# Optimization experiments

Measured on AMD Instinct MI355X. Metric: run time of the kernel, lower is better.

## Reference

```python
import jax, jax.numpy as jnp
import numpy as np

B, S, H = 4, 1024, 1024
NH, HD = 16, 64  # num heads, head dim


def setup_inputs() -> dict:
    key = jax.random.key(0)
    ks = jax.random.split(key, 7)
    scale = 1.0 / np.sqrt(H)
    return {
        "hidden_states": jax.random.normal(ks[0], (B, S, H), jnp.float32),
        "attention_mask": jnp.zeros((B, 1, 1, S), jnp.float32),
        "Wq": jax.random.normal(ks[1], (H, H), jnp.float32) * scale,
        "bq": jnp.zeros((H,), jnp.float32),
        "Wk": jax.random.normal(ks[2], (H, H), jnp.float32) * scale,
        "bk": jnp.zeros((H,), jnp.float32),
        "Wv": jax.random.normal(ks[3], (H, H), jnp.float32) * scale,
        "bv": jnp.zeros((H,), jnp.float32),
    }


def _heads(x):
    # [B,S,H] -> [B,NH,S,HD]
    return x.reshape(x.shape[0], x.shape[1], NH, HD).transpose(0, 2, 1, 3)


def reference(hidden_states, attention_mask, Wq, bq, Wk, bk, Wv, bv):
    q = _heads(hidden_states @ Wq + bq)  # [B,NH,S,HD]
    k = _heads(hidden_states @ Wk + bk)
    v = _heads(hidden_states @ Wv + bv)
    scores = jnp.einsum("bhqd,bhkd->bhqk", q, k) / np.sqrt(HD)
    scores = scores + attention_mask  # broadcast additive mask
    probs = jax.nn.softmax(scores, axis=-1)  # dropout p=0 (eval)
    ctx = jnp.einsum("bhqk,bhkd->bhqd", probs, v)
    # [B,NH,S,HD] -> [B,S,H]
    return ctx.transpose(0, 2, 1, 3).reshape(hidden_states.shape[0], hidden_states.shape[1], NH * HD)
```

## Files before the change

### kernel.cpp

```cpp
#include <hip/hip_runtime.h>
#include <hip/hip_bf16.h>

typedef __bf16 bf16_t;
typedef __bf16 bf16x8 __attribute__((ext_vector_type(8)));
typedef float f32x4 __attribute__((ext_vector_type(4)));
typedef float f32x8 __attribute__((ext_vector_type(8)));
typedef float f32x16 __attribute__((ext_vector_type(16)));
typedef unsigned uint2v __attribute__((ext_vector_type(2)));

#define MFMA16(a, b, c) __builtin_amdgcn_mfma_f32_16x16x32_bf16((a), (b), (c), 0, 0, 0)
#define MFMA32(a, b, c) __builtin_amdgcn_mfma_f32_32x32x16_bf16((a), (b), (c), 0, 0, 0)

static constexpr int BB = 4, SS = 1024, HH = 1024, NHEAD = 16, HDIM = 64;
static constexpr int MM = BB * SS;

__device__ __forceinline__ void gload_lds16(const void* g, void* l) {
  __builtin_amdgcn_global_load_lds((const __attribute__((address_space(1))) void*)g,
                                   (__attribute__((address_space(3))) void*)l, 16, 0, 0);
}

#if __has_builtin(__builtin_amdgcn_permlane32_swap)
#define PSWAP(a, b)                                                    \
  {                                                                    \
    uint2v _r = __builtin_amdgcn_permlane32_swap((a), (b), false, false); \
    (a) = _r.x;                                                        \
    (b) = _r.y;                                                        \
  }
#else
#define PSWAP(a, b) asm("v_permlane32_swap_b32 %0, %1" : "+v"(a), "+v"(b))
#endif

__device__ __forceinline__ float EXP2(float x) {
  float r;
  asm("v_exp_f32 %0, %1" : "=v"(r) : "v"(x));
  return r;
}

__global__ __launch_bounds__(256) void prep_kernel(const float* __restrict__ hs,
                                                   const float* __restrict__ Wq,
                                                   const float* __restrict__ Wk,
                                                   const float* __restrict__ Wv,
                                                   bf16_t* __restrict__ hiddenB,
                                                   bf16_t* __restrict__ WT) {
  const int t = threadIdx.x;
  if (blockIdx.x < 2048) {
    int i = (blockIdx.x * 256 + t) * 8;
    float4 a = *(const float4*)(hs + i);
    float4 b = *(const float4*)(hs + i + 4);
    union { int4 i4; bf16_t h[8]; } u;
    u.h[0] = (bf16_t)a.x; u.h[1] = (bf16_t)a.y; u.h[2] = (bf16_t)a.z; u.h[3] = (bf16_t)a.w;
    u.h[4] = (bf16_t)b.x; u.h[5] = (bf16_t)b.y; u.h[6] = (bf16_t)b.z; u.h[7] = (bf16_t)b.w;
    *(int4*)(hiddenB + i) = u.i4;
  } else {
    __shared__ float tile[32][33];
    int id = blockIdx.x - 2048;
    int z = id >> 10;
    int rem = id & 1023;
    int bx = rem & 31, by = rem >> 5;
    const float* W = (z == 0) ? Wq : (z == 1) ? Wk : Wv;
    bf16_t* Out = WT + (size_t)z * HH * HH;
    int tx = t & 31, ty = t >> 5;
    int x0 = bx * 32;
    int y0 = by * 32;
    for (int j = ty; j < 32; j += 8)
      tile[j][tx] = W[(size_t)(y0 + j) * HH + x0 + tx];
    __syncthreads();
    for (int j = ty; j < 32; j += 8)
      Out[(size_t)(x0 + j) * HH + y0 + tx] = (bf16_t)tile[tx][j];
  }
}

#define BMT 128
#define BNT 384
#define BKT 64
#define NTL 16
#define BUFBYTES 65536

__global__ __launch_bounds__(512, 2) void qkv_gemm3(const bf16_t* __restrict__ hiddenB,
                                                    const bf16_t* __restrict__ WT,
                                                    const float* __restrict__ bq,
                                                    const float* __restrict__ bk,
                                                    const float* __restrict__ bv,
                                                    bf16_t* __restrict__ Qo,
                                                    bf16_t* __restrict__ Ko,
                                                    bf16_t* __restrict__ Vt) {
  __shared__ bf16_t smem[2 * BUFBYTES / 2];

  const int wg = blockIdx.x;
  const int id = (wg & 7) * 32 + (wg >> 3);
  const int nb = id & 7;
  const int mb = id >> 3;

  const int t = threadIdx.x;
  const int lane = t & 63;
  const int w = t >> 6;
  const int wr = w >> 2;
  const int wc = w & 3;
  const int lr = lane & 15;
  const int g4 = lane >> 4;

  const unsigned schunk = (((unsigned)(t & 7)) ^ ((unsigned)((t >> 3) & 7))) << 4;
  const char* Ag = (const char*)hiddenB + (size_t)(mb * BMT) * 2048;
  const char* Bg = (const char*)WT + (size_t)(nb * BNT) * 2048;

  auto stage = [&](const char* gb, int growbase, int kbyte, char* ldsdest) {
    gload_lds16(gb + (size_t)(growbase + (t >> 3)) * 2048 + kbyte + schunk,
                ldsdest + w * 1024);
  };
  auto stage_tile = [&](int kt, char* Sb) {
    const int kb = kt * 128;
    stage(Ag, 0, kb, Sb);
    stage(Ag, 64, kb, Sb + 8192);
#pragma unroll
    for (int i = 0; i < 6; ++i) stage(Bg, i * 64, kb, Sb + 16384 + i * 8192);
  };
  const unsigned axor = ((unsigned)(lr & 7)) << 4;

  f32x4 acc[4][6] = {};

  stage_tile(0, (char*)smem);
  stage_tile(1, (char*)smem + BUFBYTES);
  asm volatile("s_waitcnt vmcnt(8)" ::: "memory");
  __builtin_amdgcn_s_barrier();

  for (int j = 0; j < NTL; ++j) {
    const char* Ab = (const char*)smem + (j & 1) * BUFBYTES;
    const char* Bb = Ab + 16384;

    bf16x8 af[4][2], bfr[6][2];
#pragma unroll
    for (int mi = 0; mi < 4; ++mi)
#pragma unroll
      for (int ks = 0; ks < 2; ++ks)
        af[mi][ks] = *(const bf16x8*)(Ab + (size_t)(wr * 64 + mi * 16 + lr) * 128 +
                                      (((unsigned)(ks * 64 + g4 * 16)) ^ axor));
#pragma unroll
    for (int ni = 0; ni < 6; ++ni)
#pragma unroll
      for (int ks = 0; ks < 2; ++ks)
        bfr[ni][ks] = *(const bf16x8*)(Bb + (size_t)(wc * 96 + ni * 16 + lr) * 128 +
                                       (((unsigned)(ks * 64 + g4 * 16)) ^ axor));

    asm volatile("s_waitcnt lgkmcnt(0)" ::: "memory");
    __builtin_amdgcn_sched_barrier(0);
    __builtin_amdgcn_s_barrier();

    if (j + 2 < NTL) stage_tile(j + 2, (char*)smem + (j & 1) * BUFBYTES);

    __builtin_amdgcn_s_setprio(1);
#pragma unroll
    for (int mi = 0; mi < 4; ++mi)
#pragma unroll
      for (int ni = 0; ni < 6; ++ni)
#pragma unroll
        for (int ks = 0; ks < 2; ++ks)
          acc[mi][ni] = MFMA16(af[mi][ks], bfr[ni][ks], acc[mi][ni]);
    __builtin_amdgcn_s_setprio(0);

    if (j + 1 < NTL) {
      if (j + 2 < NTL)
        asm volatile("s_waitcnt vmcnt(8)" ::: "memory");
      else
        asm volatile("s_waitcnt vmcnt(0)" ::: "memory");
      __builtin_amdgcn_s_barrier();
    }
  }

#pragma unroll
  for (int ni = 0; ni < 6; ++ni) {
    int col = nb * BNT + wc * 96 + ni * 16 + lr;
    int z = col >> 10;
    int ci = col & 1023;
    const float* bias = (z == 0) ? bq : (z == 1) ? bk : bv;
    float bia = bias[ci];
    int hh = ci >> 6, d = ci & 63;
    if (z < 2) {
      bf16_t* Out = (z == 0) ? Qo : Ko;
#pragma unroll
      for (int mi = 0; mi < 4; ++mi) {
#pragma unroll
        for (int r = 0; r < 4; ++r) {
          int row = mb * BMT + wr * 64 + mi * 16 + g4 * 4 + r;
          int b = row >> 10, s = row & 1023;
          Out[((size_t)(b * NHEAD + hh) * SS + s) * HDIM + d] = (bf16_t)(acc[mi][ni][r] + bia);
        }
      }
    } else {
#pragma unroll
      for (int mi = 0; mi < 4; ++mi) {
        int row0 = mb * BMT + wr * 64 + mi * 16 + g4 * 4;
        int b = row0 >> 10, s0 = row0 & 1023;
        float v0 = acc[mi][ni][0] + bia, v1 = acc[mi][ni][1] + bia;
        float v2 = acc[mi][ni][2] + bia, v3 = acc[mi][ni][3] + bia;
        unsigned u0, u1;
        asm("v_cvt_pk_bf16_f32 %0, %1, %2" : "=v"(u0) : "v"(v0), "v"(v1));
        asm("v_cvt_pk_bf16_f32 %0, %1, %2" : "=v"(u1) : "v"(v2), "v"(v3));
        uint2 pv; pv.x = u0; pv.y = u1;
        *(uint2*)&Vt[((size_t)(b * NHEAD + hh) * HDIM + d) * SS + s0] = pv;
      }
    }
  }
}

__global__ __launch_bounds__(512, 4) void attn8_kernel(const bf16_t* __restrict__ Q,
                                                       const bf16_t* __restrict__ K,
                                                       const bf16_t* __restrict__ Vt,
                                                       const float* __restrict__ mask,
                                                       float* __restrict__ out) {
  __shared__ bf16_t KVsm[2][2][2][64 * 64];
  __shared__ float Msm[SS];

  const int wg = blockIdx.x;
  const int id = (wg & 7) * 64 + (wg >> 3);
  const int xblk = id & 7;
  const int bh = id >> 3;

  const int b = bh >> 4;
  const int h = bh & 15;
  const int t = threadIdx.x;
  const int lane = t & 63;
  const int w = t >> 6;
  const int wl = w & 3;
  const int half = w >> 2;
  const int l31 = lane & 31;
  const int hi = lane >> 5;
  const int q0 = xblk * 128 + wl * 32;
  const int kvbase = half * 512;

  const bf16_t* Qh = Q + (size_t)bh * SS * HDIM;
  const bf16_t* Kh = K + (size_t)bh * SS * HDIM;
  const bf16_t* Vh = Vt + (size_t)bh * HDIM * SS;

  const float L2E = 1.4426950408889634f;
  if (t < 256) {
    float4 mv = *(const float4*)&mask[(size_t)b * SS + t * 4];
    mv.x = mv.x * L2E - 16.f; mv.y = mv.y * L2E - 16.f;
    mv.z = mv.z * L2E - 16.f; mv.w = mv.w * L2E - 16.f;
    *(float4*)&Msm[t * 4] = mv;
  }

  bf16x8 qb[4];
#pragma unroll
  for (int c = 0; c < 4; ++c) {
    bf16x8 q = *(const bf16x8*)&Qh[(size_t)(q0 + l31) * HDIM + c * 16 + hi * 8];
#pragma unroll
    for (int e = 0; e < 8; ++e) q[e] = (bf16_t)((float)q[e] * (0.125f * L2E));
    qb[c] = q;
  }

  const int srow = lane >> 3;
  const unsigned gcol = ((lane & 7) * 16) ^ (srow << 4);
  const unsigned swz = (unsigned)((l31 & 7) << 4);

  auto stageKV = [&](int tile, int buf) {
    const int kv0 = kvbase + tile * 64;
#pragma unroll
    for (int i = 0; i < 2; ++i) {
      int rbase = wl * 16 + i * 8;
      gload_lds16((const char*)Kh + (size_t)(kv0 + rbase + srow) * 128 + gcol,
                  (char*)&KVsm[half][buf][0][0] + (size_t)rbase * 128);
      gload_lds16((const char*)Vh + (size_t)(rbase + srow) * 2048 + (size_t)kv0 * 2 + gcol,
                  (char*)&KVsm[half][buf][1][0] + (size_t)rbase * 128);
    }
  };

  f32x16 acc0 = {}, acc1 = {};
  f32x8 la = {}, lb = {};

  stageKV(0, 0);
  asm volatile("s_waitcnt vmcnt(0) lgkmcnt(0)" ::: "memory");
  __builtin_amdgcn_s_barrier();

  for (int tt = 0; tt < 8; ++tt) {
    if (tt + 1 < 8) stageKV(tt + 1, (tt + 1) & 1);
    const char* Kb = (const char*)&KVsm[half][tt & 1][0][0];
    const char* Vb = (const char*)&KVsm[half][tt & 1][1][0];
    const int kv0 = kvbase + tt * 64;

    f32x16 st0 = {}, st1 = {};
    __builtin_amdgcn_s_setprio(1);
#pragma unroll
    for (int c = 0; c < 4; ++c) {
      bf16x8 kf0 = *(const bf16x8*)(Kb + (size_t)l31 * 128 + ((unsigned)(c * 32 + hi * 16) ^ swz));
      st0 = MFMA32(kf0, qb[c], st0);
    }
#pragma unroll
    for (int c = 0; c < 4; ++c) {
      bf16x8 kf1 = *(const bf16x8*)(Kb + (size_t)(32 + l31) * 128 + ((unsigned)(c * 32 + hi * 16) ^ swz));
      st1 = MFMA32(kf1, qb[c], st1);
    }
    __builtin_amdgcn_s_setprio(0);

#pragma unroll
    for (int k2 = 0; k2 < 8; ++k2) {
      int off = 8 * (k2 >> 1) + 4 * hi + 2 * (k2 & 1);
      float2 m0v = *(const float2*)&Msm[kv0 + off];
      float2 m1v = *(const float2*)&Msm[kv0 + 32 + off];
      st0[2 * k2] += m0v.x; st0[2 * k2 + 1] += m0v.y;
      st1[2 * k2] += m1v.x; st1[2 * k2 + 1] += m1v.y;
    }
#pragma unroll
    for (int r = 0; r < 16; ++r) st0[r] = EXP2(st0[r]);
#pragma unroll
    for (int r = 0; r < 16; ++r) st1[r] = EXP2(st1[r]);

#pragma unroll
    for (int r = 0; r < 8; ++r) {
      la[r] += st0[r] + st0[r + 8];
      lb[r] += st1[r] + st1[r + 8];
    }

    unsigned wd0[8], wd1[8];
#pragma unroll
    for (int k2 = 0; k2 < 8; ++k2) {
      unsigned r0, r1;
      float a0f = st0[2 * k2], a1f = st0[2 * k2 + 1];
      float b0f = st1[2 * k2], b1f = st1[2 * k2 + 1];
      asm("v_cvt_pk_bf16_f32 %0, %1, %2" : "=v"(r0) : "v"(a0f), "v"(a1f));
      asm("v_cvt_pk_bf16_f32 %0, %1, %2" : "=v"(r1) : "v"(b0f), "v"(b1f));
      wd0[k2] = r0; wd1[k2] = r1;
    }
    unsigned a0 = wd0[0], b0 = wd0[2]; PSWAP(a0, b0);
    unsigned a1 = wd0[1], b1 = wd0[3]; PSWAP(a1, b1);
    unsigned a2 = wd0[4], b2 = wd0[6]; PSWAP(a2, b2);
    unsigned a3 = wd0[5], b3 = wd0[7]; PSWAP(a3, b3);
    unsigned c0 = wd1[0], d0 = wd1[2]; PSWAP(c0, d0);
    unsigned c1 = wd1[1], d1 = wd1[3]; PSWAP(c1, d1);
    unsigned c2 = wd1[4], d2 = wd1[6]; PSWAP(c2, d2);
    unsigned c3 = wd1[5], d3 = wd1[7]; PSWAP(c3, d3);
    union { unsigned u[4]; bf16x8 v; } pf0, pf1, pf2, pf3;
    pf0.u[0] = a0; pf0.u[1] = a1; pf0.u[2] = b0; pf0.u[3] = b1;
    pf1.u[0] = a2; pf1.u[1] = a3; pf1.u[2] = b2; pf1.u[3] = b3;
    pf2.u[0] = c0; pf2.u[1] = c1; pf2.u[2] = d0; pf2.u[3] = d1;
    pf3.u[0] = c2; pf3.u[1] = c3; pf3.u[2] = d2; pf3.u[3] = d3;

    __builtin_amdgcn_s_setprio(1);
    {
      bf16x8 vf;
      vf = *(const bf16x8*)(Vb + (size_t)(l31) * 128 + ((unsigned)(0 * 32 + hi * 16) ^ swz));
      acc0 = MFMA32(vf, pf0.v, acc0);
      vf = *(const bf16x8*)(Vb + (size_t)(32 + l31) * 128 + ((unsigned)(0 * 32 + hi * 16) ^ swz));
      acc1 = MFMA32(vf, pf0.v, acc1);
      vf = *(const bf16x8*)(Vb + (size_t)(l31) * 128 + ((unsigned)(1 * 32 + hi * 16) ^ swz));
      acc0 = MFMA32(vf, pf1.v, acc0);
      vf = *(const bf16x8*)(Vb + (size_t)(32 + l31) * 128 + ((unsigned)(1 * 32 + hi * 16) ^ swz));
      acc1 = MFMA32(vf, pf1.v, acc1);
      vf = *(const bf16x8*)(Vb + (size_t)(l31) * 128 + ((unsigned)(2 * 32 + hi * 16) ^ swz));
      acc0 = MFMA32(vf, pf2.v, acc0);
      vf = *(const bf16x8*)(Vb + (size_t)(32 + l31) * 128 + ((unsigned)(2 * 32 + hi * 16) ^ swz));
      acc1 = MFMA32(vf, pf2.v, acc1);
      vf = *(const bf16x8*)(Vb + (size_t)(l31) * 128 + ((unsigned)(3 * 32 + hi * 16) ^ swz));
      acc0 = MFMA32(vf, pf3.v, acc0);
      vf = *(const bf16x8*)(Vb + (size_t)(32 + l31) * 128 + ((unsigned)(3 * 32 + hi * 16) ^ swz));
      acc1 = MFMA32(vf, pf3.v, acc1);
    }
    __builtin_amdgcn_s_setprio(0);

    asm volatile("s_waitcnt vmcnt(0)" ::: "memory");
    __builtin_amdgcn_s_barrier();
  }

  float l_run;
  {
    float s0 = (la[0] + lb[0]) + (la[1] + lb[1]);
    float s1 = (la[2] + lb[2]) + (la[3] + lb[3]);
    float s2 = (la[4] + lb[4]) + (la[5] + lb[5]);
    float s3 = (la[6] + lb[6]) + (la[7] + lb[7]);
    l_run = (s0 + s1) + (s2 + s3);
    l_run += __shfl_xor(l_run, 32);
  }

  __syncthreads();
  float* mb = (float*)&KVsm[0][0][0][0];
  if (half == 1) {
    float* dst = mb + ((size_t)(wl * 64 + lane)) * 36;
#pragma unroll
    for (int g = 0; g < 4; ++g) {
      float4 w0, w1;
      w0.x = acc0[g * 4 + 0]; w0.y = acc0[g * 4 + 1];
      w0.z = acc0[g * 4 + 2]; w0.w = acc0[g * 4 + 3];
      w1.x = acc1[g * 4 + 0]; w1.y = acc1[g * 4 + 1];
      w1.z = acc1[g * 4 + 2]; w1.w = acc1[g * 4 + 3];
      *(float4*)(dst + g * 4) = w0;
      *(float4*)(dst + 16 + g * 4) = w1;
    }
    dst[32] = l_run;
  }
  __syncthreads();
  if (half == 0) {
    const float* src = mb + ((size_t)(wl * 64 + lane)) * 36;
    float rinv = 1.0f / (l_run + src[32]);
    int q = q0 + l31;
    float* ob = out + ((size_t)(b * SS + q)) * HH + h * HDIM;
#pragma unroll
    for (int g = 0; g < 4; ++g) {
      float4 o0, o1;
      o0.x = (acc0[g * 4 + 0] + src[g * 4 + 0]) * rinv;
      o0.y = (acc0[g * 4 + 1] + src[g * 4 + 1]) * rinv;
      o0.z = (acc0[g * 4 + 2] + src[g * 4 + 2]) * rinv;
      o0.w = (acc0[g * 4 + 3] + src[g * 4 + 3]) * rinv;
      o1.x = (acc1[g * 4 + 0] + src[16 + g * 4 + 0]) * rinv;
      o1.y = (acc1[g * 4 + 1] + src[16 + g * 4 + 1]) * rinv;
      o1.z = (acc1[g * 4 + 2] + src[16 + g * 4 + 2]) * rinv;
      o1.w = (acc1[g * 4 + 3] + src[16 + g * 4 + 3]) * rinv;
      *(float4*)&ob[g * 8 + 4 * hi] = o0;
      *(float4*)&ob[32 + g * 8 + 4 * hi] = o1;
    }
  }
}

extern "C" void kernel_launch(void* const* d_in, const int* in_sizes, int n_in,
                              void* d_out, int out_size, void* d_ws, size_t ws_size,
                              hipStream_t stream) {
  const float* hs   = (const float*)d_in[0];
  const float* mask = (const float*)d_in[1];
  const float* Wq   = (const float*)d_in[2];
  const float* bq   = (const float*)d_in[3];
  const float* Wk   = (const float*)d_in[4];
  const float* bk   = (const float*)d_in[5];
  const float* Wv   = (const float*)d_in[6];
  const float* bv   = (const float*)d_in[7];
  float* out = (float*)d_out;

  char* ws = (char*)d_ws;
  bf16_t* hiddenB = (bf16_t*)ws;
  bf16_t* WT      = (bf16_t*)(ws + (size_t)8 * 1024 * 1024);
  bf16_t* Qb      = (bf16_t*)(ws + (size_t)14 * 1024 * 1024);
  bf16_t* Kb      = (bf16_t*)(ws + (size_t)22 * 1024 * 1024);
  bf16_t* Vt      = (bf16_t*)(ws + (size_t)30 * 1024 * 1024);

  prep_kernel<<<2048 + 3072, 256, 0, stream>>>(hs, Wq, Wk, Wv, hiddenB, WT);
  qkv_gemm3<<<256, 512, 0, stream>>>(hiddenB, WT, bq, bk, bv, Qb, Kb, Vt);
  attn8_kernel<<<512, 512, 0, stream>>>(Qb, Kb, Vt, mask, out);
}
```

Baseline: 74.04 us.

## Split QKV GEMM k-step into three phases interleaving LDS reads, staging, and MFMA

Restructures the QKV projection GEMM main loop into three sub-phases. Each phase reads a third of the B fragments from LDS, issues part of the next tile's global-to-LDS loads after a barrier, then runs MFMAs on that slice. The B column mapping per wave changes so each phase covers a 128-column band, and the epilogue is remapped to match. The aim is to overlap LDS reads, global prefetch and MFMA work more finely and to lower register pressure from holding all B fragments at once, at the cost of three barriers per k-step instead of one.

```diff
diff --git a/kernel.cpp b/kernel.cpp
--- a/kernel.cpp
+++ b/kernel.cpp
@@ -76,7 +76,7 @@
 #define NTL 16
 #define BUFBYTES 65536
 
-__global__ __launch_bounds__(512, 2) void qkv_gemm3(const bf16_t* __restrict__ hiddenB,
+__global__ __launch_bounds__(512, 2) void qkv_gemm5(const bf16_t* __restrict__ hiddenB,
                                                     const bf16_t* __restrict__ WT,
                                                     const float* __restrict__ bq,
                                                     const float* __restrict__ bk,
@@ -107,58 +107,108 @@
     gload_lds16(gb + (size_t)(growbase + (t >> 3)) * 2048 + kbyte + schunk,
                 ldsdest + w * 1024);
   };
-  auto stage_tile = [&](int kt, char* Sb) {
-    const int kb = kt * 128;
-    stage(Ag, 0, kb, Sb);
-    stage(Ag, 64, kb, Sb + 8192);
-#pragma unroll
-    for (int i = 0; i < 6; ++i) stage(Bg, i * 64, kb, Sb + 16384 + i * 8192);
+  const unsigned axor = ((unsigned)(lr & 7)) << 4;
+
+  auto rdA = [&](const char* Ab, int mi, int ks) -> bf16x8 {
+    return *(const bf16x8*)(Ab + (size_t)(wr * 64 + mi * 16 + lr) * 128 +
+                            (((unsigned)(ks * 64 + g4 * 16)) ^ axor));
   };
-  const unsigned axor = ((unsigned)(lr & 7)) << 4;
+  auto rdB = [&](const char* Bb, int p, int ni, int ks) -> bf16x8 {
+    return *(const bf16x8*)(Bb + (size_t)(p * 128 + wc * 32 + ni * 16 + lr) * 128 +
+                            (((unsigned)(ks * 64 + g4 * 16)) ^ axor));
+  };
 
   f32x4 acc[4][6] = {};
 
-  stage_tile(0, (char*)smem);
-  stage_tile(1, (char*)smem + BUFBYTES);
+  {
+    char* S0 = (char*)smem;
+    stage(Ag, 0, 0, S0); stage(Ag, 64, 0, S0 + 8192);
+#pragma unroll
+    for (int i = 0; i < 6; ++i) stage(Bg, i * 64, 0, S0 + 16384 + i * 8192);
+    char* S1 = (char*)smem + BUFBYTES;
+    stage(Ag, 0, 128, S1); stage(Ag, 64, 128, S1 + 8192);
+#pragma unroll
+    for (int i = 0; i < 6; ++i) stage(Bg, i * 64, 128, S1 + 16384 + i * 8192);
+  }
   asm volatile("s_waitcnt vmcnt(8)" ::: "memory");
   __builtin_amdgcn_s_barrier();
 
   for (int j = 0; j < NTL; ++j) {
     const char* Ab = (const char*)smem + (j & 1) * BUFBYTES;
     const char* Bb = Ab + 16384;
-
-    bf16x8 af[4][2], bfr[6][2];
+    char* Sb = (char*)smem + (j & 1) * BUFBYTES;
+    const bool st = (j + 2 < NTL);
+    const int kb2 = (j + 2) * 128;
+
+    bf16x8 af[4][2], b0[2][2];
 #pragma unroll
     for (int mi = 0; mi < 4; ++mi)
 #pragma unroll
-      for (int ks = 0; ks < 2; ++ks)
-        af[mi][ks] = *(const bf16x8*)(Ab + (size_t)(wr * 64 + mi * 16 + lr) * 128 +
-                                      (((unsigned)(ks * 64 + g4 * 16)) ^ axor));
-#pragma unroll
-    for (int ni = 0; ni < 6; ++ni)
-#pragma unroll
-      for (int ks = 0; ks < 2; ++ks)
-        bfr[ni][ks] = *(const bf16x8*)(Bb + (size_t)(wc * 96 + ni * 16 + lr) * 128 +
-                                       (((unsigned)(ks * 64 + g4 * 16)) ^ axor));
-
+      for (int ks = 0; ks < 2; ++ks) af[mi][ks] = rdA(Ab, mi, ks);
+#pragma unroll
+    for (int ni = 0; ni < 2; ++ni)
+#pragma unroll
+      for (int ks = 0; ks < 2; ++ks) b0[ni][ks] = rdB(Bb, 0, ni, ks);
     asm volatile("s_waitcnt lgkmcnt(0)" ::: "memory");
-    __builtin_amdgcn_sched_barrier(0);
     __builtin_amdgcn_s_barrier();
-
-    if (j + 2 < NTL) stage_tile(j + 2, (char*)smem + (j & 1) * BUFBYTES);
-
+    if (st) {
+      stage(Ag, 0, kb2, Sb); stage(Ag, 64, kb2, Sb + 8192);
+      stage(Bg, 0, kb2, Sb + 16384); stage(Bg, 64, kb2, Sb + 16384 + 8192);
+    }
     __builtin_amdgcn_s_setprio(1);
 #pragma unroll
     for (int mi = 0; mi < 4; ++mi)
 #pragma unroll
-      for (int ni = 0; ni < 6; ++ni)
+      for (int ni = 0; ni < 2; ++ni)
 #pragma unroll
         for (int ks = 0; ks < 2; ++ks)
-          acc[mi][ni] = MFMA16(af[mi][ks], bfr[ni][ks], acc[mi][ni]);
+          acc[mi][ni] = MFMA16(af[mi][ks], b0[ni][ks], acc[mi][ni]);
     __builtin_amdgcn_s_setprio(0);
 
+    bf16x8 b1[2][2];
+#pragma unroll
+    for (int ni = 0; ni < 2; ++ni)
+#pragma unroll
+      for (int ks = 0; ks < 2; ++ks) b1[ni][ks] = rdB(Bb, 1, ni, ks);
+    asm volatile("s_waitcnt lgkmcnt(0)" ::: "memory");
+    __builtin_amdgcn_s_barrier();
+    if (st) {
+      stage(Bg, 128, kb2, Sb + 16384 + 2 * 8192);
+      stage(Bg, 192, kb2, Sb + 16384 + 3 * 8192);
+    }
+    __builtin_amdgcn_s_setprio(1);
+#pragma unroll
+    for (int mi = 0; mi < 4; ++mi)
+#pragma unroll
+      for (int ni = 0; ni < 2; ++ni)
+#pragma unroll
+        for (int ks = 0; ks < 2; ++ks)
+          acc[mi][2 + ni] = MFMA16(af[mi][ks], b1[ni][ks], acc[mi][2 + ni]);
+    __builtin_amdgcn_s_setprio(0);
+
+    bf16x8 b2[2][2];
+#pragma unroll
+    for (int ni = 0; ni < 2; ++ni)
+#pragma unroll
+      for (int ks = 0; ks < 2; ++ks) b2[ni][ks] = rdB(Bb, 2, ni, ks);
+    asm volatile("s_waitcnt lgkmcnt(0)" ::: "memory");
+    __builtin_amdgcn_s_barrier();
+    if (st) {
+      stage(Bg, 256, kb2, Sb + 16384 + 4 * 8192);
+      stage(Bg, 320, kb2, Sb + 16384 + 5 * 8192);
+    }
+    __builtin_amdgcn_s_setprio(1);
+#pragma unroll
+    for (int mi = 0; mi < 4; ++mi)
+#pragma unroll
+      for (int ni = 0; ni < 2; ++ni)
+#pragma unroll
+        for (int ks = 0; ks < 2; ++ks)
+          acc[mi][4 + ni] = MFMA16(af[mi][ks], b2[ni][ks], acc[mi][4 + ni]);
+    __builtin_amdgcn_s_setprio(0);
+
     if (j + 1 < NTL) {
-      if (j + 2 < NTL)
+      if (st)
         asm volatile("s_waitcnt vmcnt(8)" ::: "memory");
       else
         asm volatile("s_waitcnt vmcnt(0)" ::: "memory");
@@ -167,8 +217,9 @@
   }
 
 #pragma unroll
-  for (int ni = 0; ni < 6; ++ni) {
-    int col = nb * BNT + wc * 96 + ni * 16 + lr;
+  for (int ni6 = 0; ni6 < 6; ++ni6) {
+    int p = ni6 >> 1, ni = ni6 & 1;
+    int col = nb * BNT + p * 128 + wc * 32 + ni * 16 + lr;
     int z = col >> 10;
     int ci = col & 1023;
     const float* bias = (z == 0) ? bq : (z == 1) ? bk : bv;
@@ -182,7 +233,7 @@
         for (int r = 0; r < 4; ++r) {
           int row = mb * BMT + wr * 64 + mi * 16 + g4 * 4 + r;
           int b = row >> 10, s = row & 1023;
-          Out[((size_t)(b * NHEAD + hh) * SS + s) * HDIM + d] = (bf16_t)(acc[mi][ni][r] + bia);
+          Out[((size_t)(b * NHEAD + hh) * SS + s) * HDIM + d] = (bf16_t)(acc[mi][ni6][r] + bia);
         }
       }
     } else {
@@ -190,8 +241,8 @@
       for (int mi = 0; mi < 4; ++mi) {
         int row0 = mb * BMT + wr * 64 + mi * 16 + g4 * 4;
         int b = row0 >> 10, s0 = row0 & 1023;
-        float v0 = acc[mi][ni][0] + bia, v1 = acc[mi][ni][1] + bia;
-        float v2 = acc[mi][ni][2] + bia, v3 = acc[mi][ni][3] + bia;
+        float v0 = acc[mi][ni6][0] + bia, v1 = acc[mi][ni6][1] + bia;
+        float v2 = acc[mi][ni6][2] + bia, v3 = acc[mi][ni6][3] + bia;
         unsigned u0, u1;
         asm("v_cvt_pk_bf16_f32 %0, %1, %2" : "=v"(u0) : "v"(v0), "v"(v1));
         asm("v_cvt_pk_bf16_f32 %0, %1, %2" : "=v"(u1) : "v"(v2), "v"(v3));
@@ -430,6 +481,6 @@
   bf16_t* Vt      = (bf16_t*)(ws + (size_t)30 * 1024 * 1024);
 
   prep_kernel<<<2048 + 3072, 256, 0, stream>>>(hs, Wq, Wk, Wv, hiddenB, WT);
-  qkv_gemm3<<<256, 512, 0, stream>>>(hiddenB, WT, bq, bk, bv, Qb, Kb, Vt);
+  qkv_gemm5<<<256, 512, 0, stream>>>(hiddenB, WT, bq, bk, bv, Qb, Kb, Vt);
   attn8_kernel<<<512, 512, 0, stream>>>(Qb, Kb, Vt, mask, out);
 }
```

Result: faster. 70.79 us (-4.4%).
